# Kernel optimization log

Hardware: AMD Instinct MI355X
Metric: run time of the kernel (lower is better)

The kernel has to match this reference:

```python
import jax, jax.numpy as jnp
import numpy as np
import math
from jax import lax

L, E, H, F = 4, 1024, 16, 4096
B, S = 8, 512
VV, VR = 40, 30
DIST_V = 200
PAD_ID = 0


def setup_inputs() -> dict:
    key = jax.random.key(0)
    ks = iter(jax.random.split(key, 32))
    w = lambda *sh: jax.random.normal(next(ks), sh, jnp.float32) * 0.02
    inp = {
        'val_emb': w(VV, E),
        'ring_emb': w(VR, E),
        'dist_emb': w(DIST_V, H),
        'Wqkv': w(L, 3 * E, E), 'bqkv': jnp.zeros((L, 3 * E), jnp.float32),
        'Wo': w(L, E, E), 'bo': jnp.zeros((L, E), jnp.float32),
        'ln1_s': jnp.ones((L, E), jnp.float32), 'ln1_b': jnp.zeros((L, E), jnp.float32),
        'W1': w(L, F, E), 'b1': jnp.zeros((L, F), jnp.float32),
        'W2': w(L, E, F), 'b2': jnp.zeros((L, E), jnp.float32),
        'ln2_s': jnp.ones((L, E), jnp.float32), 'ln2_b': jnp.zeros((L, E), jnp.float32),
        'lnf_s': jnp.ones((E,), jnp.float32), 'lnf_b': jnp.zeros((E,), jnp.float32),
        'gen_W': w(VV * VR, E), 'gen_b': jnp.zeros((VV * VR,), jnp.float32),
    }
    val = jax.random.randint(next(ks), (B, S), 0, VV)
    val = val.at[:, 0].set(1)  # ensure first key is never <pad> (id 0)
    inp['val_sequences'] = val
    inp['ring_sequences'] = jax.random.randint(next(ks), (B, S), 0, VR)
    inp['distance_squares'] = jax.random.randint(next(ks), (B, S, S), 0, DIST_V)
    return inp


def _ln(x, s, b):
    m = x.mean(-1, keepdims=True)
    v = ((x - m) ** 2).mean(-1, keepdims=True)
    return (x - m) / jnp.sqrt(v + 1e-5) * s + b


def _forward(val_emb, ring_emb, dist_emb, Wqkv, bqkv, Wo, bo, ln1_s, ln1_b,
             W1, b1, W2, b2, ln2_s, ln2_b, lnf_s, lnf_b, gen_W, gen_b,
             val_sequences, ring_sequences, distance_squares):
    Bv, Sv = val_sequences.shape
    dh = E // H
    scale = 1.0 / math.sqrt(dh)
    # token embeddings, each scaled by sqrt(emb_size)
    x = (val_emb[val_sequences] + ring_emb[ring_sequences]) * math.sqrt(E)  # [B,S,E]
    # distance bias [B,S,S,H] -> [B,H,S,S], causal fill with -inf, key padding -inf
    bias = jnp.transpose(dist_emb[distance_squares], (0, 3, 1, 2))
    causal = jnp.tril(jnp.ones((Sv, Sv), bool))
    mask = jnp.where(causal[None, None], bias, -jnp.inf)
    pad = (val_sequences == PAD_ID)  # [B,S]
    mask = jnp.where(pad[:, None, None, :], -jnp.inf, mask)

    def step(h, p):
        wqkv, bq, wo, bo_, l1s, l1b, w1, b1_, w2, b2_, l2s, l2b = p
        qkv = h @ wqkv.T + bq  # [B,S,3E]
        q, k, v = jnp.split(qkv, 3, axis=-1)
        q = q.reshape(Bv, Sv, H, dh).transpose(0, 2, 1, 3)
        k = k.reshape(Bv, Sv, H, dh).transpose(0, 2, 1, 3)
        v = v.reshape(Bv, Sv, H, dh).transpose(0, 2, 1, 3)
        scores = jnp.einsum('bhqd,bhkd->bhqk', q, k) * scale + mask
        a = jax.nn.softmax(scores, axis=-1)
        ctx = jnp.einsum('bhqk,bhkd->bhqd', a, v)
        ctx = ctx.transpose(0, 2, 1, 3).reshape(Bv, Sv, E)
        h = _ln(h + ctx @ wo.T + bo_, l1s, l1b)  # post-norm
        ff = jax.nn.gelu(h @ w1.T + b1_, approximate=False) @ w2.T + b2_
        h = _ln(h + ff, l2s, l2b)
        return h, None

    layer_params = (Wqkv, bqkv, Wo, bo, ln1_s, ln1_b, W1, b1, W2, b2, ln2_s, ln2_b)
    x, _ = lax.scan(step, x, layer_params)
    x = _ln(x, lnf_s, lnf_b)
    return x @ gen_W.T + gen_b  # [B,S,VV*VR]


def reference(val_emb, ring_emb, dist_emb, Wqkv, bqkv, Wo, bo, ln1_s, ln1_b,
              W1, b1, W2, b2, ln2_s, ln2_b, lnf_s, lnf_b, gen_W, gen_b,
              val_sequences, ring_sequences, distance_squares):
    return _forward(val_emb, ring_emb, dist_emb, Wqkv, bqkv, Wo, bo, ln1_s, ln1_b,
                    W1, b1, W2, b2, ln2_s, ln2_b, lnf_s, lnf_b, gen_W, gen_b,
                    val_sequences, ring_sequences, distance_squares)
```

## Files before the change

### kernel.cpp

```cpp
#include <hip/hip_runtime.h>
#include <hip/hip_bf16.h>

typedef __attribute__((ext_vector_type(8))) short bf16x8;
typedef __attribute__((ext_vector_type(4))) float f32x4;
typedef unsigned short u16;
typedef __attribute__((ext_vector_type(4))) unsigned short u16x4;

#define L_ 4
#define E_ 1024
#define H_ 16
#define F_ 4096
#define B_ 8
#define S_ 512
#define T_ 4096
#define GEN_N 1200

#define AS1 __attribute__((address_space(1)))
#define AS3 __attribute__((address_space(3)))

static __device__ __forceinline__ u16 f2bf(float f) {
  unsigned u = __float_as_uint(f);
  unsigned r = (u + 0x7fffu + ((u >> 16) & 1u)) >> 16;
  return (u16)r;
}

static __device__ __forceinline__ float fast_gelu(float v) {
  float y = 0.7978845608f * (v + 0.044715f * v * v * v);
  y = fminf(fmaxf(y, -9.f), 9.f);
  float e2 = __expf(2.f * y);
  float th = (e2 - 1.f) / (e2 + 1.f);
  return 0.5f * v * (1.f + th);
}

__global__ __launch_bounds__(256) void cvt_bf16(const float* __restrict__ src,
                                                u16* __restrict__ dst, int n) {
  int i = (blockIdx.x * 256 + threadIdx.x) * 4;
  if (i >= n) return;
  float4 v = *reinterpret_cast<const float4*>(src + i);
  u16x4 o = {f2bf(v.x), f2bf(v.y), f2bf(v.z), f2bf(v.w)};
  *reinterpret_cast<u16x4*>(dst + i) = o;
}

__global__ __launch_bounds__(256) void embed_k(const float* __restrict__ val_emb,
                                               const float* __restrict__ ring_emb,
                                               const int* __restrict__ vseq,
                                               const int* __restrict__ rseq,
                                               float* __restrict__ h, u16* __restrict__ xbf) {
  int tok = blockIdx.x;
  int e = threadIdx.x * 4;
  int v = vseq[tok], r = rseq[tok];
  float4 a = *reinterpret_cast<const float4*>(val_emb + v * E_ + e);
  float4 b = *reinterpret_cast<const float4*>(ring_emb + r * E_ + e);
  float4 o;
  o.x = (a.x + b.x) * 32.f; o.y = (a.y + b.y) * 32.f;
  o.z = (a.z + b.z) * 32.f; o.w = (a.w + b.w) * 32.f;
  *reinterpret_cast<float4*>(h + (size_t)tok * E_ + e) = o;
  u16x4 ob = {f2bf(o.x), f2bf(o.y), f2bf(o.z), f2bf(o.w)};
  *reinterpret_cast<u16x4*>(xbf + (size_t)tok * E_ + e) = ob;
}

__global__ __launch_bounds__(256) void ln_k(const float* hin, const float* add0,
                                            const float* add1, const float* cbias,
                                            const float* g, const float* bta,
                                            float* hout, u16* xout) {
  int tok = blockIdx.x;
  int e = threadIdx.x * 4;
  float4 v = *reinterpret_cast<const float4*>(hin + (size_t)tok * E_ + e);
  if (add0) {
    float4 a0 = *reinterpret_cast<const float4*>(add0 + (size_t)tok * E_ + e);
    float4 a1 = *reinterpret_cast<const float4*>(add1 + (size_t)tok * E_ + e);
    float4 cb = *reinterpret_cast<const float4*>(cbias + e);
    v.x += a0.x + a1.x + cb.x; v.y += a0.y + a1.y + cb.y;
    v.z += a0.z + a1.z + cb.z; v.w += a0.w + a1.w + cb.w;
  }
  float s = v.x + v.y + v.z + v.w;
  float q = v.x * v.x + v.y * v.y + v.z * v.z + v.w * v.w;
  #pragma unroll
  for (int off = 1; off < 64; off <<= 1) {
    s += __shfl_xor(s, off, 64);
    q += __shfl_xor(q, off, 64);
  }
  __shared__ float ls[4], lq[4];
  int wv = threadIdx.x >> 6, ln = threadIdx.x & 63;
  if (ln == 0) { ls[wv] = s; lq[wv] = q; }
  __syncthreads();
  s = ls[0] + ls[1] + ls[2] + ls[3];
  q = lq[0] + lq[1] + lq[2] + lq[3];
  float mean = s * (1.f / E_);
  float var = q * (1.f / E_) - mean * mean;
  float inv = rsqrtf(var + 1e-5f);
  float4 gg = *reinterpret_cast<const float4*>(g + e);
  float4 bb = *reinterpret_cast<const float4*>(bta + e);
  float4 o;
  o.x = (v.x - mean) * inv * gg.x + bb.x;
  o.y = (v.y - mean) * inv * gg.y + bb.y;
  o.z = (v.z - mean) * inv * gg.z + bb.z;
  o.w = (v.w - mean) * inv * gg.w + bb.w;
  if (hout) *reinterpret_cast<float4*>(hout + (size_t)tok * E_ + e) = o;
  u16x4 ob = {f2bf(o.x), f2bf(o.y), f2bf(o.z), f2bf(o.w)};
  *reinterpret_cast<u16x4*>(xout + (size_t)tok * E_ + e) = ob;
}

template <int EPI, int NW, int SPLITK>
__global__ __launch_bounds__(512, 2) void gemm_big(const u16* __restrict__ A,
                                                   const u16* __restrict__ W,
                                                   const float* __restrict__ bias,
                                                   void* __restrict__ Cp,
                                                   int M, int N, int K, int tilesN) {
  constexpr int BN = 64 * NW;
  __shared__ __align__(16) u16 As[2][256 * 64];
  __shared__ __align__(16) u16 Bs[2][BN * 64];
  int tid = threadIdx.x;
  int wid = tid >> 6, ln = tid & 63;
  int wm = wid >> 2, wn = wid & 3;
  int lr = ln & 15, lk = ln >> 4;
  int nwg = gridDim.x;
  int bid = blockIdx.x;
  int swz = ((nwg & 7) == 0) ? ((bid & 7) * (nwg >> 3) + (bid >> 3)) : bid;
  int sp = 0, tile = swz;
  if (SPLITK > 1) { sp = swz & (SPLITK - 1); tile = swz / SPLITK; }
  int tm = tile / tilesN, tn = tile % tilesN;
  int row0 = tm * 256, col0 = tn * BN;
  int Ks = K / SPLITK;
  int kbase = sp * Ks;

  int srow = tid >> 3;
  int schunk = ((tid & 7) ^ (srow & 7)) * 8;
  const u16* gA = A + (size_t)(row0 + srow) * K + kbase + schunk;
  const u16* gB = W + (size_t)(col0 + srow) * K + kbase + schunk;
  size_t ldsBase = (size_t)((wid << 3) * 64) * 2;

  auto stage = [&](int buf, int kt) {
    size_t ko = (size_t)kt * 64;
    #pragma unroll
    for (int i = 0; i < 4; ++i)
      __builtin_amdgcn_global_load_lds(
          (const AS1 void*)(gA + (size_t)i * 64 * K + ko),
          (AS3 void*)((char*)&As[buf][0] + ldsBase + (size_t)i * 64 * 128), 16, 0, 0);
    #pragma unroll
    for (int i = 0; i < NW; ++i)
      __builtin_amdgcn_global_load_lds(
          (const AS1 void*)(gB + (size_t)i * 64 * K + ko),
          (AS3 void*)((char*)&Bs[buf][0] + ldsBase + (size_t)i * 64 * 128), 16, 0, 0);
  };

  f32x4 acc[8][NW];
  f32x4 z = {0.f, 0.f, 0.f, 0.f};
  #pragma unroll
  for (int m = 0; m < 8; ++m)
    #pragma unroll
    for (int n = 0; n < NW; ++n) acc[m][n] = z;

  auto compute = [&](int buf) {
    #pragma unroll
    for (int s = 0; s < 2; ++s) {
      int ch = ((s * 4 + lk) ^ (lr & 7)) * 8;
      bf16x8 bfr[NW];
      #pragma unroll
      for (int n = 0; n < NW; ++n)
        bfr[n] = *reinterpret_cast<const bf16x8*>(&Bs[buf][(wn * (16 * NW) + n * 16 + lr) * 64 + ch]);
      #pragma unroll
      for (int m = 0; m < 8; ++m) {
        bf16x8 af = *reinterpret_cast<const bf16x8*>(&As[buf][(wm * 128 + m * 16 + lr) * 64 + ch]);
        #pragma unroll
        for (int n = 0; n < NW; ++n)
          acc[m][n] = __builtin_amdgcn_mfma_f32_16x16x32_bf16(af, bfr[n], acc[m][n], 0, 0, 0);
      }
    }
  };

  int nt = Ks >> 6;
  stage(0, 0);
  int cur = 0;
  for (int t = 0; t < nt; ++t) {
    if (t + 1 < nt) {
      stage(cur ^ 1, t + 1);
      if constexpr (NW == 2) asm volatile("s_waitcnt vmcnt(6)" ::: "memory");
      else if constexpr (NW == 3) asm volatile("s_waitcnt vmcnt(7)" ::: "memory");
      else asm volatile("s_waitcnt vmcnt(8)" ::: "memory");
    } else {
      asm volatile("s_waitcnt vmcnt(0)" ::: "memory");
    }
    __builtin_amdgcn_s_barrier();
    asm volatile("" ::: "memory");
    compute(cur);
    asm volatile("" ::: "memory");
    __builtin_amdgcn_s_barrier();
    cur ^= 1;
  }

  #pragma unroll
  for (int n = 0; n < NW; ++n) {
    int col = col0 + wn * (16 * NW) + n * 16 + lr;
    float bv = (EPI == 2) ? 0.f : bias[col];
    #pragma unroll
    for (int m = 0; m < 8; ++m) {
      int rbase = row0 + wm * 128 + m * 16 + lk * 4;
      #pragma unroll
      for (int r2 = 0; r2 < 4; ++r2) {
        float v = acc[m][n][r2] + bv;
        if (EPI == 1) v = fast_gelu(v);
        if (EPI == 2)
          ((float*)Cp)[(size_t)sp * M * N + (size_t)(rbase + r2) * N + col] = v;
        else
          ((u16*)Cp)[(size_t)(rbase + r2) * N + col] = f2bf(v);
      }
    }
  }
}

template <int EPI>
__global__ __launch_bounds__(256) void gemm_bt(const u16* __restrict__ A,
                                               const u16* __restrict__ W,
                                               const float* __restrict__ bias,
                                               void* __restrict__ Cp,
                                               int M, int N, int K, int tilesN) {
  __shared__ __align__(16) u16 As[3][128 * 32];
  __shared__ __align__(16) u16 Bs[3][128 * 32];
  int tid = threadIdx.x;
  int wv = tid >> 6, ln = tid & 63;
  int wm = wv >> 1, wn = wv & 1;
  int nwg = gridDim.x;
  int bid = blockIdx.x;
  int swz = ((nwg & 7) == 0) ? ((bid & 7) * (nwg >> 3) + (bid >> 3)) : bid;
  int tm = swz / tilesN, tn = swz % tilesN;
  int row0 = tm * 128, col0 = tn * 128;
  int lr = ln & 15, lk = ln >> 4;

  f32x4 acc[4][4];
  f32x4 z = {0.f, 0.f, 0.f, 0.f};
  #pragma unroll
  for (int m = 0; m < 4; ++m)
    #pragma unroll
    for (int n = 0; n < 4; ++n) acc[m][n] = z;

  int srow = tid >> 2;
  int scol = ((tid & 3) ^ (srow & 3)) * 8;
  const u16* gA0 = A + (size_t)(row0 + srow) * K + scol;
  const u16* gA1 = A + (size_t)(row0 + 64 + srow) * K + scol;
  int wr0 = col0 + srow;      if (wr0 >= N) wr0 = N - 1;
  int wr1 = col0 + 64 + srow; if (wr1 >= N) wr1 = N - 1;
  const u16* gB0 = W + (size_t)wr0 * K + scol;
  const u16* gB1 = W + (size_t)wr1 * K + scol;
  size_t ldsOff0 = (size_t)(wv << 6) * 16;
  size_t ldsOff1 = (size_t)(256 + (wv << 6)) * 16;

  auto stage = [&](int buf, int k0) {
    __builtin_amdgcn_global_load_lds((const AS1 void*)(gA0 + k0),
        (AS3 void*)((char*)&As[buf][0] + ldsOff0), 16, 0, 0);
    __builtin_amdgcn_global_load_lds((const AS1 void*)(gB0 + k0),
        (AS3 void*)((char*)&Bs[buf][0] + ldsOff0), 16, 0, 0);
    __builtin_amdgcn_global_load_lds((const AS1 void*)(gA1 + k0),
        (AS3 void*)((char*)&As[buf][0] + ldsOff1), 16, 0, 0);
    __builtin_amdgcn_global_load_lds((const AS1 void*)(gB1 + k0),
        (AS3 void*)((char*)&Bs[buf][0] + ldsOff1), 16, 0, 0);
  };

  int ck = (lk ^ (lr & 3)) * 8;
  auto compute = [&](int buf) {
    bf16x8 af[4], bfr[4];
    #pragma unroll
    for (int m = 0; m < 4; ++m)
      af[m] = *reinterpret_cast<const bf16x8*>(&As[buf][(wm * 64 + m * 16 + lr) * 32 + ck]);
    #pragma unroll
    for (int n = 0; n < 4; ++n)
      bfr[n] = *reinterpret_cast<const bf16x8*>(&Bs[buf][(wn * 64 + n * 16 + lr) * 32 + ck]);
    #pragma unroll
    for (int m = 0; m < 4; ++m)
      #pragma unroll
      for (int n = 0; n < 4; ++n)
        acc[m][n] = __builtin_amdgcn_mfma_f32_16x16x32_bf16(af[m], bfr[n], acc[m][n], 0, 0, 0);
  };

  int nsteps = K >> 5;
  stage(0, 0);
  stage(1, 32);
  int bt = 0;
  for (int t = 0; t < nsteps; ++t) {
    int rem = nsteps - 1 - t;
    if (rem >= 2) {
      int b2 = (bt == 0) ? 2 : bt - 1;
      stage(b2, (t + 2) << 5);
      asm volatile("s_waitcnt vmcnt(8)" ::: "memory");
    } else if (rem == 1) {
      asm volatile("s_waitcnt vmcnt(4)" ::: "memory");
    } else {
      asm volatile("s_waitcnt vmcnt(0)" ::: "memory");
    }
    __builtin_amdgcn_s_barrier();
    asm volatile("" ::: "memory");
    compute(bt);
    asm volatile("" ::: "memory");
    __builtin_amdgcn_s_barrier();
    bt = (bt == 2) ? 0 : bt + 1;
  }

  #pragma unroll
  for (int n = 0; n < 4; ++n) {
    int col = col0 + wn * 64 + n * 16 + lr;
    if (col >= N) continue;
    float bv = bias[col];
    #pragma unroll
    for (int m = 0; m < 4; ++m) {
      int rbase = row0 + wm * 64 + m * 16 + lk * 4;
      #pragma unroll
      for (int r2 = 0; r2 < 4; ++r2) {
        float v = acc[m][n][r2] + bv;
        int row = rbase + r2;
        if (EPI == 2)
          ((float*)Cp)[(size_t)row * N + col] = v;
        else
          ((float*)Cp)[(size_t)row * N + col] += v;
      }
    }
  }
}

__global__ __launch_bounds__(256) void vtrans_k(const u16* __restrict__ qkv,
                                                u16* __restrict__ Vt) {
  int blk = blockIdx.x;
  int kt = blk & 7, bh = blk >> 3;
  int b = bh >> 4, h = bh & 15;
  __shared__ u16 t[64 * 66];
  int tid = threadIdx.x;
  #pragma unroll
  for (int i = 0; i < 16; ++i) {
    int idx = i * 256 + tid;
    int kk = idx >> 6, d = idx & 63;
    t[kk * 66 + d] = qkv[(size_t)(b * S_ + kt * 64 + kk) * 3072 + 2 * E_ + h * 64 + d];
  }
  __syncthreads();
  #pragma unroll
  for (int i = 0; i < 16; ++i) {
    int idx = i * 256 + tid;
    int d = idx >> 6, kk = idx & 63;
    Vt[(size_t)(bh * 64 + d) * S_ + kt * 64 + kk] = t[kk * 66 + d];
  }
}

__global__ __launch_bounds__(256, 4) void attn_scores_k(const u16* __restrict__ qkv,
                                                        const int* __restrict__ dist,
                                                        const float* __restrict__ dist_emb,
                                                        const int* __restrict__ vseq,
                                                        u16* __restrict__ P,
                                                        float* __restrict__ invl) {
  int blk = blockIdx.x;
  int bh = blk & 127;
  int qt = blk >> 7;
  int b = bh >> 4, h = bh & 15;
  int tid = threadIdx.x, wv = tid >> 6, ln = tid & 63;
  int lr = ln & 15, lk = ln >> 4;

  __shared__ float de[208];
  __shared__ unsigned char padf[512];
  __shared__ unsigned char d8[64 * 512];

  int ncol = (qt + 1) * 64;
  for (int i = tid; i < 208; i += 256)
    de[i] = (i < 200) ? dist_emb[i * H_ + h] : -1e30f;
  for (int i = tid; i < (ncol >> 2); i += 256) {
    int4 v = *reinterpret_cast<const int4*>(vseq + b * S_ + i * 4);
    uchar4 pz;
    pz.x = (v.x == 0); pz.y = (v.y == 0); pz.z = (v.z == 0); pz.w = (v.w == 0);
    *reinterpret_cast<uchar4*>(&padf[i * 4]) = pz;
  }
  __syncthreads();

  {
    int r = tid >> 2;
    const int* drow = dist + ((size_t)(b * S_ + qt * 64 + r) << 9);
    int nc4 = ncol >> 2;
    for (int c4 = (tid & 3); c4 < nc4; c4 += 4) {
      int4 dv = *reinterpret_cast<const int4*>(drow + c4 * 4);
      uchar4 o;
      o.x = padf[c4 * 4 + 0] ? (unsigned char)200 : (unsigned char)dv.x;
      o.y = padf[c4 * 4 + 1] ? (unsigned char)200 : (unsigned char)dv.y;
      o.z = padf[c4 * 4 + 2] ? (unsigned char)200 : (unsigned char)dv.z;
      o.w = padf[c4 * 4 + 3] ? (unsigned char)200 : (unsigned char)dv.w;
      *reinterpret_cast<uchar4*>(&d8[(r << 9) + c4 * 4]) = o;
    }
  }
  __syncthreads();

  int q0 = qt * 64 + wv * 16;
  int nv = 4 * qt + wv + 1;
  int nreq = 4 * qt + 2 * (wv >> 1) + 2;
  int qrow = q0 + lk * 4;
  int lrow = wv * 16 + lk * 4;

  bf16x8 aq0 = *reinterpret_cast<const bf16x8*>(
      qkv + (size_t)(b * S_ + q0 + lr) * 3072 + h * 64 + lk * 8);
  bf16x8 aq1 = *reinterpret_cast<const bf16x8*>(
      qkv + (size_t)(b * S_ + q0 + lr) * 3072 + h * 64 + 32 + lk * 8);

  float sm[4] = {0.f, 0.f, 0.f, 0.f};
  f32x4 z = {0.f, 0.f, 0.f, 0.f};
  int nch = (nv + 3) >> 2;
  #pragma unroll 1
  for (int c = 0; c < nch; ++c) {
    int base = c * 4;
    f32x4 acc[4] = {z, z, z, z};
    #pragma unroll
    for (int j = 0; j < 4; ++j) {
      int n = base + j;
      if (n < nv) {
        const u16* kb = qkv + (size_t)(b * S_ + n * 16 + lr) * 3072 + E_ + h * 64 + lk * 8;
        bf16x8 bk0 = *reinterpret_cast<const bf16x8*>(kb);
        bf16x8 bk1 = *reinterpret_cast<const bf16x8*>(kb + 32);
        acc[j] = __builtin_amdgcn_mfma_f32_16x16x32_bf16(aq0, bk0, acc[j], 0, 0, 0);
        acc[j] = __builtin_amdgcn_mfma_f32_16x16x32_bf16(aq1, bk1, acc[j], 0, 0, 0);
      }
    }
    #pragma unroll
    for (int j = 0; j < 4; ++j) {
      int n = base + j;
      if (n < nv) {
        int col = n * 16 + lr;
        #pragma unroll
        for (int r2 = 0; r2 < 4; ++r2) {
          float e = 0.f;
          if (col <= qrow + r2) {
            int d = d8[((lrow + r2) << 9) + col];
            e = __expf(acc[j][r2] * 0.125f + de[d]);
          }
          sm[r2] += e;
          P[(size_t)(bh * S_ + qrow + r2) * S_ + col] = f2bf(e);
        }
      }
    }
  }
  for (int n = nv; n < nreq; ++n) {
    int col = n * 16 + lr;
    #pragma unroll
    for (int r2 = 0; r2 < 4; ++r2)
      P[(size_t)(bh * S_ + qrow + r2) * S_ + col] = 0;
  }
  #pragma unroll
  for (int off = 1; off < 16; off <<= 1)
    #pragma unroll
    for (int r2 = 0; r2 < 4; ++r2) sm[r2] += __shfl_xor(sm[r2], off, 64);
  if (lr == 0) {
    #pragma unroll
    for (int r2 = 0; r2 < 4; ++r2)
      invl[bh * S_ + qrow + r2] = 1.f / sm[r2];
  }
}

__global__ __launch_bounds__(256) void attn_pv_k(const u16* __restrict__ P,
                                                 const u16* __restrict__ Vt,
                                                 const float* __restrict__ invl,
                                                 u16* __restrict__ ctx) {
  int blk = blockIdx.x;
  int mt = blk & 3, bh = blk >> 2;
  int b = bh >> 4, h = bh & 15;
  int tid = threadIdx.x, wv = tid >> 6, ln = tid & 63;
  int lr = ln & 15, lk = ln >> 4;
  int r0 = mt * 128 + wv * 32;
  f32x4 acc[2][4];
  f32x4 z = {0.f, 0.f, 0.f, 0.f};
  #pragma unroll
  for (int m = 0; m < 2; ++m)
    #pragma unroll
    for (int n = 0; n < 4; ++n) acc[m][n] = z;
  int nks = mt * 4 + wv + 1;
  for (int ks = 0; ks < nks; ++ks) {
    int k0 = ks * 32;
    bf16x8 ap[2];
    #pragma unroll
    for (int m = 0; m < 2; ++m)
      ap[m] = *reinterpret_cast<const bf16x8*>(
          P + (size_t)(bh * S_ + r0 + m * 16 + lr) * S_ + k0 + lk * 8);
    #pragma unroll
    for (int n = 0; n < 4; ++n) {
      bf16x8 bv = *reinterpret_cast<const bf16x8*>(
          Vt + (size_t)(bh * 64 + n * 16 + lr) * S_ + k0 + lk * 8);
      #pragma unroll
      for (int m = 0; m < 2; ++m)
        acc[m][n] = __builtin_amdgcn_mfma_f32_16x16x32_bf16(ap[m], bv, acc[m][n], 0, 0, 0);
    }
  }
  float il[2][4];
  #pragma unroll
  for (int m = 0; m < 2; ++m)
    #pragma unroll
    for (int r = 0; r < 4; ++r)
      il[m][r] = invl[bh * S_ + r0 + m * 16 + lk * 4 + r];
  #pragma unroll
  for (int m = 0; m < 2; ++m)
    #pragma unroll
    for (int n = 0; n < 4; ++n)
      #pragma unroll
      for (int r = 0; r < 4; ++r) {
        int row = r0 + m * 16 + lk * 4 + r;
        int col = n * 16 + lr;
        ctx[(size_t)(b * S_ + row) * E_ + h * 64 + col] = f2bf(acc[m][n][r] * il[m][r]);
      }
}

extern "C" void kernel_launch(void* const* d_in, const int* in_sizes, int n_in,
                              void* d_out, int out_size, void* d_ws, size_t ws_size,
                              hipStream_t stream) {
  const float* val_emb = (const float*)d_in[0];
  const float* ring_emb = (const float*)d_in[1];
  const float* dist_emb = (const float*)d_in[2];
  const float* Wqkv = (const float*)d_in[3];
  const float* bqkv = (const float*)d_in[4];
  const float* Wo = (const float*)d_in[5];
  const float* bo = (const float*)d_in[6];
  const float* ln1_s = (const float*)d_in[7];
  const float* ln1_b = (const float*)d_in[8];
  const float* W1 = (const float*)d_in[9];
  const float* b1 = (const float*)d_in[10];
  const float* W2 = (const float*)d_in[11];
  const float* b2 = (const float*)d_in[12];
  const float* ln2_s = (const float*)d_in[13];
  const float* ln2_b = (const float*)d_in[14];
  const float* lnf_s = (const float*)d_in[15];
  const float* lnf_b = (const float*)d_in[16];
  const float* gen_W = (const float*)d_in[17];
  const float* gen_b = (const float*)d_in[18];
  const int* vseq = (const int*)d_in[19];
  const int* rseq = (const int*)d_in[20];
  const int* dist = (const int*)d_in[21];

  char* ws = (char*)d_ws;
  size_t off = 0;
  auto alloc = [&](size_t nbytes) {
    char* p = ws + off;
    off += (nbytes + 255) & ~(size_t)255;
    return p;
  };
  u16* gw_bf = (u16*)alloc((size_t)GEN_N * E_ * 2);
  u16* wqkv_l = (u16*)alloc((size_t)3 * E_ * E_ * 2);
  u16* wo_l = (u16*)alloc((size_t)E_ * E_ * 2);
  u16* w1_l = (u16*)alloc((size_t)F_ * E_ * 2);
  u16* w2_l = (u16*)alloc((size_t)E_ * F_ * 2);
  float* h = (float*)alloc((size_t)T_ * E_ * 4);
  u16* x_bf = (u16*)alloc((size_t)T_ * E_ * 2);
  u16* qkv_bf = (u16*)alloc((size_t)T_ * 3 * E_ * 2);
  u16* ctx_bf = (u16*)alloc((size_t)T_ * E_ * 2);
  u16* vt_bf = (u16*)alloc((size_t)B_ * H_ * 64 * S_ * 2);
  float* invl = (float*)alloc((size_t)B_ * H_ * S_ * 4);
  u16* p_bf = (u16*)alloc((size_t)B_ * H_ * S_ * S_ * 2);
  u16* ff_bf = p_bf;
  float* psum = (float*)(p_bf + (size_t)T_ * F_);
  (void)ws_size; (void)in_sizes; (void)n_in; (void)out_size; (void)rseq;

  auto cvt = [&](const float* s, u16* d, int n) {
    cvt_bf16<<<dim3((n / 4 + 255) / 256), dim3(256), 0, stream>>>(s, d, n);
  };
  cvt(gen_W, gw_bf, GEN_N * E_);

  embed_k<<<dim3(T_), dim3(256), 0, stream>>>(val_emb, ring_emb, vseq, rseq, h, x_bf);

  for (int l = 0; l < L_; ++l) {
    cvt(Wqkv + (size_t)l * 3 * E_ * E_, wqkv_l, 3 * E_ * E_);
    cvt(Wo + (size_t)l * E_ * E_, wo_l, E_ * E_);
    cvt(W1 + (size_t)l * F_ * E_, w1_l, F_ * E_);
    cvt(W2 + (size_t)l * E_ * F_, w2_l, E_ * F_);

    gemm_big<0, 3, 1><<<dim3(256), dim3(512), 0, stream>>>(
        x_bf, wqkv_l, bqkv + (size_t)l * 3 * E_, qkv_bf, T_, 3 * E_, E_, 16);
    vtrans_k<<<dim3(B_ * H_ * 8), dim3(256), 0, stream>>>(qkv_bf, vt_bf);
    attn_scores_k<<<dim3(B_ * H_ * 8), dim3(256), 0, stream>>>(qkv_bf, dist, dist_emb, vseq,
                                                               p_bf, invl);
    attn_pv_k<<<dim3(B_ * H_ * 4), dim3(256), 0, stream>>>(p_bf, vt_bf, invl, ctx_bf);
    gemm_bt<3><<<dim3(32 * 8), dim3(256), 0, stream>>>(
        ctx_bf, wo_l, bo + (size_t)l * E_, h, T_, E_, E_, 8);
    ln_k<<<dim3(T_), dim3(256), 0, stream>>>(h, nullptr, nullptr, nullptr,
                                             ln1_s + (size_t)l * E_, ln1_b + (size_t)l * E_,
                                             h, x_bf);
    gemm_big<1, 4, 1><<<dim3(256), dim3(512), 0, stream>>>(
        x_bf, w1_l, b1 + (size_t)l * F_, ff_bf, T_, F_, E_, 16);
    gemm_big<2, 2, 2><<<dim3(256), dim3(512), 0, stream>>>(
        ff_bf, w2_l, nullptr, psum, T_, E_, F_, 8);
    ln_k<<<dim3(T_), dim3(256), 0, stream>>>(h, psum, psum + (size_t)T_ * E_,
                                             b2 + (size_t)l * E_,
                                             ln2_s + (size_t)l * E_, ln2_b + (size_t)l * E_,
                                             h, x_bf);
  }
  ln_k<<<dim3(T_), dim3(256), 0, stream>>>(h, nullptr, nullptr, nullptr, lnf_s, lnf_b,
                                           nullptr, x_bf);
  gemm_bt<2><<<dim3(32 * 10), dim3(256), 0, stream>>>(
      x_bf, gw_bf, gen_b, (float*)d_out, T_, GEN_N, E_, 10);
}
```

Baseline: 1.161 ms.

## Switch GEMM to 4-stage BK=32 LDS pipeline with priority boost

The main GEMM goes from a double-buffered pipeline with K-tiles of 64 to a 4-buffer ring with K-tiles of 32, keeping three loads in flight ahead of compute. The LDS swizzle and the staging layout are reworked for 32-wide rows, and the vmcnt waits are adjusted per stage. s_setprio is raised around the MFMA compute. The aim is to hide global-load latency better, at the cost of twice as many barriers per unit of K and more complex wait accounting. For NW==3, half the waves issue the second B load, so the vmcnt counts differ between waves, which could be fragile.

New measurement: 1.268 ms. 1.09x slower.

```diff
diff --git a/kernel.cpp b/kernel.cpp
--- a/kernel.cpp
+++ b/kernel.cpp
@@ -108,8 +108,8 @@
                                                    void* __restrict__ Cp,
                                                    int M, int N, int K, int tilesN) {
   constexpr int BN = 64 * NW;
-  __shared__ __align__(16) u16 As[2][256 * 64];
-  __shared__ __align__(16) u16 Bs[2][BN * 64];
+  __shared__ __align__(16) u16 As[4][256 * 32];
+  __shared__ __align__(16) u16 Bs[4][BN * 32];
   int tid = threadIdx.x;
   int wid = tid >> 6, ln = tid & 63;
   int wm = wid >> 2, wn = wid & 3;
@@ -124,24 +124,28 @@
   int Ks = K / SPLITK;
   int kbase = sp * Ks;
 
-  int srow = tid >> 3;
-  int schunk = ((tid & 7) ^ (srow & 7)) * 8;
-  const u16* gA = A + (size_t)(row0 + srow) * K + kbase + schunk;
-  const u16* gB = W + (size_t)(col0 + srow) * K + kbase + schunk;
-  size_t ldsBase = (size_t)((wid << 3) * 64) * 2;
+  int srow = tid >> 2;
+  int sch = ((tid & 3) ^ ((srow >> 1) & 3)) * 8;
+  const u16* gA = A + (size_t)(row0 + srow) * K + kbase + sch;
+  const u16* gB = W + (size_t)(col0 + srow) * K + kbase + sch;
+  size_t wslot = (size_t)wid * 1024;
 
   auto stage = [&](int buf, int kt) {
-    size_t ko = (size_t)kt * 64;
-    #pragma unroll
-    for (int i = 0; i < 4; ++i)
-      __builtin_amdgcn_global_load_lds(
-          (const AS1 void*)(gA + (size_t)i * 64 * K + ko),
-          (AS3 void*)((char*)&As[buf][0] + ldsBase + (size_t)i * 64 * 128), 16, 0, 0);
-    #pragma unroll
-    for (int i = 0; i < NW; ++i)
-      __builtin_amdgcn_global_load_lds(
-          (const AS1 void*)(gB + (size_t)i * 64 * K + ko),
-          (AS3 void*)((char*)&Bs[buf][0] + ldsBase + (size_t)i * 64 * 128), 16, 0, 0);
+    size_t ko = (size_t)kt * 32;
+    __builtin_amdgcn_global_load_lds((const AS1 void*)(gA + ko),
+        (AS3 void*)((char*)&As[buf][0] + wslot), 16, 0, 0);
+    __builtin_amdgcn_global_load_lds((const AS1 void*)(gA + (size_t)128 * K + ko),
+        (AS3 void*)((char*)&As[buf][0] + 8192 + wslot), 16, 0, 0);
+    __builtin_amdgcn_global_load_lds((const AS1 void*)(gB + ko),
+        (AS3 void*)((char*)&Bs[buf][0] + wslot), 16, 0, 0);
+    if constexpr (NW == 4) {
+      __builtin_amdgcn_global_load_lds((const AS1 void*)(gB + (size_t)128 * K + ko),
+          (AS3 void*)((char*)&Bs[buf][0] + 8192 + wslot), 16, 0, 0);
+    } else if constexpr (NW == 3) {
+      if (wid < 4)
+        __builtin_amdgcn_global_load_lds((const AS1 void*)(gB + (size_t)128 * K + ko),
+            (AS3 void*)((char*)&Bs[buf][0] + 8192 + wslot), 16, 0, 0);
+    }
   };
 
   f32x4 acc[8][NW];
@@ -151,42 +155,48 @@
     #pragma unroll
     for (int n = 0; n < NW; ++n) acc[m][n] = z;
 
+  int ck = (lk ^ ((lr >> 1) & 3)) * 8;
   auto compute = [&](int buf) {
-    #pragma unroll
-    for (int s = 0; s < 2; ++s) {
-      int ch = ((s * 4 + lk) ^ (lr & 7)) * 8;
-      bf16x8 bfr[NW];
+    bf16x8 bfr[NW];
+    #pragma unroll
+    for (int n = 0; n < NW; ++n)
+      bfr[n] = *reinterpret_cast<const bf16x8*>(&Bs[buf][(wn * (16 * NW) + n * 16 + lr) * 32 + ck]);
+    #pragma unroll
+    for (int m = 0; m < 8; ++m) {
+      bf16x8 af = *reinterpret_cast<const bf16x8*>(&As[buf][(wm * 128 + m * 16 + lr) * 32 + ck]);
       #pragma unroll
       for (int n = 0; n < NW; ++n)
-        bfr[n] = *reinterpret_cast<const bf16x8*>(&Bs[buf][(wn * (16 * NW) + n * 16 + lr) * 64 + ch]);
-      #pragma unroll
-      for (int m = 0; m < 8; ++m) {
-        bf16x8 af = *reinterpret_cast<const bf16x8*>(&As[buf][(wm * 128 + m * 16 + lr) * 64 + ch]);
-        #pragma unroll
-        for (int n = 0; n < NW; ++n)
-          acc[m][n] = __builtin_amdgcn_mfma_f32_16x16x32_bf16(af, bfr[n], acc[m][n], 0, 0, 0);
-      }
+        acc[m][n] = __builtin_amdgcn_mfma_f32_16x16x32_bf16(af, bfr[n], acc[m][n], 0, 0, 0);
     }
   };
 
-  int nt = Ks >> 6;
+  int nt = Ks >> 5;
   stage(0, 0);
-  int cur = 0;
+  stage(1, 1);
+  stage(2, 2);
   for (int t = 0; t < nt; ++t) {
-    if (t + 1 < nt) {
-      stage(cur ^ 1, t + 1);
-      if constexpr (NW == 2) asm volatile("s_waitcnt vmcnt(6)" ::: "memory");
-      else if constexpr (NW == 3) asm volatile("s_waitcnt vmcnt(7)" ::: "memory");
-      else asm volatile("s_waitcnt vmcnt(8)" ::: "memory");
+    int buf = t & 3;
+    int rem = nt - 1 - t;
+    if (rem >= 3) {
+      stage((t + 3) & 3, t + 3);
+      if constexpr (NW == 4) asm volatile("s_waitcnt vmcnt(12)" ::: "memory");
+      else asm volatile("s_waitcnt vmcnt(9)" ::: "memory");
+    } else if (rem == 2) {
+      if constexpr (NW == 4) asm volatile("s_waitcnt vmcnt(8)" ::: "memory");
+      else asm volatile("s_waitcnt vmcnt(6)" ::: "memory");
+    } else if (rem == 1) {
+      if constexpr (NW == 4) asm volatile("s_waitcnt vmcnt(4)" ::: "memory");
+      else asm volatile("s_waitcnt vmcnt(3)" ::: "memory");
     } else {
       asm volatile("s_waitcnt vmcnt(0)" ::: "memory");
     }
     __builtin_amdgcn_s_barrier();
     asm volatile("" ::: "memory");
-    compute(cur);
+    __builtin_amdgcn_s_setprio(1);
+    compute(buf);
+    __builtin_amdgcn_s_setprio(0);
     asm volatile("" ::: "memory");
     __builtin_amdgcn_s_barrier();
-    cur ^= 1;
   }
 
   #pragma unroll
```

## Fuse V transpose into QKV GEMM, unify Wo and generator GEMMs on gemm_big

Applied to the files above, without the earlier changes.

Removes the separate vtrans_k kernel by having the QKV GEMM epilogue also scatter V values into the transposed Vt buffer. Replaces gemm_bt for the Wo projection with split-K gemm_big writing partial sums that the following layernorm reduces with the bias, and runs the generator projection through gemm_big with a padded weight buffer. This cuts kernel launches and intermediate traffic. In exchange the Vt scatter stores are uncoalesced, and the padded generator weight rows (1200 to 1280) are read without the pad region being written.

After: 1.161 ms. No clear change (+0.0%).

```diff
diff --git a/kernel.cpp b/kernel.cpp
--- a/kernel.cpp
+++ b/kernel.cpp
@@ -14,6 +14,7 @@
 #define S_ 512
 #define T_ 4096
 #define GEN_N 1200
+#define GEN_PAD 1280
 
 #define AS1 __attribute__((address_space(1)))
 #define AS3 __attribute__((address_space(3)))
@@ -106,6 +107,7 @@
                                                    const u16* __restrict__ W,
                                                    const float* __restrict__ bias,
                                                    void* __restrict__ Cp,
+                                                   u16* __restrict__ Vt,
                                                    int M, int N, int K, int tilesN) {
   constexpr int BN = 64 * NW;
   __shared__ __align__(16) u16 As[2][256 * 64];
@@ -192,6 +194,7 @@
   #pragma unroll
   for (int n = 0; n < NW; ++n) {
     int col = col0 + wn * (16 * NW) + n * 16 + lr;
+    if (col >= N) continue;
     float bv = (EPI == 2) ? 0.f : bias[col];
     #pragma unroll
     for (int m = 0; m < 8; ++m) {
@@ -200,141 +203,23 @@
       for (int r2 = 0; r2 < 4; ++r2) {
         float v = acc[m][n][r2] + bv;
         if (EPI == 1) v = fast_gelu(v);
-        if (EPI == 2)
-          ((float*)Cp)[(size_t)sp * M * N + (size_t)(rbase + r2) * N + col] = v;
-        else
-          ((u16*)Cp)[(size_t)(rbase + r2) * N + col] = f2bf(v);
-      }
-    }
-  }
-}
-
-template <int EPI>
-__global__ __launch_bounds__(256) void gemm_bt(const u16* __restrict__ A,
-                                               const u16* __restrict__ W,
-                                               const float* __restrict__ bias,
-                                               void* __restrict__ Cp,
-                                               int M, int N, int K, int tilesN) {
-  __shared__ __align__(16) u16 As[3][128 * 32];
-  __shared__ __align__(16) u16 Bs[3][128 * 32];
-  int tid = threadIdx.x;
-  int wv = tid >> 6, ln = tid & 63;
-  int wm = wv >> 1, wn = wv & 1;
-  int nwg = gridDim.x;
-  int bid = blockIdx.x;
-  int swz = ((nwg & 7) == 0) ? ((bid & 7) * (nwg >> 3) + (bid >> 3)) : bid;
-  int tm = swz / tilesN, tn = swz % tilesN;
-  int row0 = tm * 128, col0 = tn * 128;
-  int lr = ln & 15, lk = ln >> 4;
-
-  f32x4 acc[4][4];
-  f32x4 z = {0.f, 0.f, 0.f, 0.f};
-  #pragma unroll
-  for (int m = 0; m < 4; ++m)
-    #pragma unroll
-    for (int n = 0; n < 4; ++n) acc[m][n] = z;
-
-  int srow = tid >> 2;
-  int scol = ((tid & 3) ^ (srow & 3)) * 8;
-  const u16* gA0 = A + (size_t)(row0 + srow) * K + scol;
-  const u16* gA1 = A + (size_t)(row0 + 64 + srow) * K + scol;
-  int wr0 = col0 + srow;      if (wr0 >= N) wr0 = N - 1;
-  int wr1 = col0 + 64 + srow; if (wr1 >= N) wr1 = N - 1;
-  const u16* gB0 = W + (size_t)wr0 * K + scol;
-  const u16* gB1 = W + (size_t)wr1 * K + scol;
-  size_t ldsOff0 = (size_t)(wv << 6) * 16;
-  size_t ldsOff1 = (size_t)(256 + (wv << 6)) * 16;
-
-  auto stage = [&](int buf, int k0) {
-    __builtin_amdgcn_global_load_lds((const AS1 void*)(gA0 + k0),
-        (AS3 void*)((char*)&As[buf][0] + ldsOff0), 16, 0, 0);
-    __builtin_amdgcn_global_load_lds((const AS1 void*)(gB0 + k0),
-        (AS3 void*)((char*)&Bs[buf][0] + ldsOff0), 16, 0, 0);
-    __builtin_amdgcn_global_load_lds((const AS1 void*)(gA1 + k0),
-        (AS3 void*)((char*)&As[buf][0] + ldsOff1), 16, 0, 0);
-    __builtin_amdgcn_global_load_lds((const AS1 void*)(gB1 + k0),
-        (AS3 void*)((char*)&Bs[buf][0] + ldsOff1), 16, 0, 0);
-  };
-
-  int ck = (lk ^ (lr & 3)) * 8;
-  auto compute = [&](int buf) {
-    bf16x8 af[4], bfr[4];
-    #pragma unroll
-    for (int m = 0; m < 4; ++m)
-      af[m] = *reinterpret_cast<const bf16x8*>(&As[buf][(wm * 64 + m * 16 + lr) * 32 + ck]);
-    #pragma unroll
-    for (int n = 0; n < 4; ++n)
-      bfr[n] = *reinterpret_cast<const bf16x8*>(&Bs[buf][(wn * 64 + n * 16 + lr) * 32 + ck]);
-    #pragma unroll
-    for (int m = 0; m < 4; ++m)
-      #pragma unroll
-      for (int n = 0; n < 4; ++n)
-        acc[m][n] = __builtin_amdgcn_mfma_f32_16x16x32_bf16(af[m], bfr[n], acc[m][n], 0, 0, 0);
-  };
-
-  int nsteps = K >> 5;
-  stage(0, 0);
-  stage(1, 32);
-  int bt = 0;
-  for (int t = 0; t < nsteps; ++t) {
-    int rem = nsteps - 1 - t;
-    if (rem >= 2) {
-      int b2 = (bt == 0) ? 2 : bt - 1;
-      stage(b2, (t + 2) << 5);
-      asm volatile("s_waitcnt vmcnt(8)" ::: "memory");
-    } else if (rem == 1) {
-      asm volatile("s_waitcnt vmcnt(4)" ::: "memory");
-    } else {
-      asm volatile("s_waitcnt vmcnt(0)" ::: "memory");
-    }
-    __builtin_amdgcn_s_barrier();
-    asm volatile("" ::: "memory");
-    compute(bt);
-    asm volatile("" ::: "memory");
-    __builtin_amdgcn_s_barrier();
-    bt = (bt == 2) ? 0 : bt + 1;
-  }
-
-  #pragma unroll
-  for (int n = 0; n < 4; ++n) {
-    int col = col0 + wn * 64 + n * 16 + lr;
-    if (col >= N) continue;
-    float bv = bias[col];
-    #pragma unroll
-    for (int m = 0; m < 4; ++m) {
-      int rbase = row0 + wm * 64 + m * 16 + lk * 4;
-      #pragma unroll
-      for (int r2 = 0; r2 < 4; ++r2) {
-        float v = acc[m][n][r2] + bv;
         int row = rbase + r2;
         if (EPI == 2)
+          ((float*)Cp)[(size_t)sp * M * N + (size_t)row * N + col] = v;
+        else if (EPI == 3)
           ((float*)Cp)[(size_t)row * N + col] = v;
-        else
-          ((float*)Cp)[(size_t)row * N + col] += v;
+        else {
+          u16 bw = f2bf(v);
+          ((u16*)Cp)[(size_t)row * N + col] = bw;
+          if (EPI == 0 && Vt != nullptr && col >= 2 * E_) {
+            int dg = col - 2 * E_;
+            int hh = dg >> 6, dd = dg & 63;
+            int bb = row >> 9, ss = row & 511;
+            Vt[((size_t)((bb * 16 + hh) * 64 + dd) << 9) + ss] = bw;
+          }
+        }
       }
     }
-  }
-}
-
-__global__ __launch_bounds__(256) void vtrans_k(const u16* __restrict__ qkv,
-                                                u16* __restrict__ Vt) {
-  int blk = blockIdx.x;
-  int kt = blk & 7, bh = blk >> 3;
-  int b = bh >> 4, h = bh & 15;
-  __shared__ u16 t[64 * 66];
-  int tid = threadIdx.x;
-  #pragma unroll
-  for (int i = 0; i < 16; ++i) {
-    int idx = i * 256 + tid;
-    int kk = idx >> 6, d = idx & 63;
-    t[kk * 66 + d] = qkv[(size_t)(b * S_ + kt * 64 + kk) * 3072 + 2 * E_ + h * 64 + d];
-  }
-  __syncthreads();
-  #pragma unroll
-  for (int i = 0; i < 16; ++i) {
-    int idx = i * 256 + tid;
-    int d = idx >> 6, kk = idx & 63;
-    Vt[(size_t)(bh * 64 + d) * S_ + kt * 64 + kk] = t[kk * 66 + d];
   }
 }
 
@@ -530,7 +415,7 @@
     off += (nbytes + 255) & ~(size_t)255;
     return p;
   };
-  u16* gw_bf = (u16*)alloc((size_t)GEN_N * E_ * 2);
+  u16* gw_bf = (u16*)alloc((size_t)GEN_PAD * E_ * 2);
   u16* wqkv_l = (u16*)alloc((size_t)3 * E_ * E_ * 2);
   u16* wo_l = (u16*)alloc((size_t)E_ * E_ * 2);
   u16* w1_l = (u16*)alloc((size_t)F_ * E_ * 2);
@@ -560,20 +445,20 @@
     cvt(W2 + (size_t)l * E_ * F_, w2_l, E_ * F_);
 
     gemm_big<0, 3, 1><<<dim3(256), dim3(512), 0, stream>>>(
-        x_bf, wqkv_l, bqkv + (size_t)l * 3 * E_, qkv_bf, T_, 3 * E_, E_, 16);
-    vtrans_k<<<dim3(B_ * H_ * 8), dim3(256), 0, stream>>>(qkv_bf, vt_bf);
+        x_bf, wqkv_l, bqkv + (size_t)l * 3 * E_, qkv_bf, vt_bf, T_, 3 * E_, E_, 16);
     attn_scores_k<<<dim3(B_ * H_ * 8), dim3(256), 0, stream>>>(qkv_bf, dist, dist_emb, vseq,
                                                                p_bf, invl);
     attn_pv_k<<<dim3(B_ * H_ * 4), dim3(256), 0, stream>>>(p_bf, vt_bf, invl, ctx_bf);
-    gemm_bt<3><<<dim3(32 * 8), dim3(256), 0, stream>>>(
-        ctx_bf, wo_l, bo + (size_t)l * E_, h, T_, E_, E_, 8);
-    ln_k<<<dim3(T_), dim3(256), 0, stream>>>(h, nullptr, nullptr, nullptr,
+    gemm_big<2, 2, 2><<<dim3(256), dim3(512), 0, stream>>>(
+        ctx_bf, wo_l, nullptr, psum, nullptr, T_, E_, E_, 8);
+    ln_k<<<dim3(T_), dim3(256), 0, stream>>>(h, psum, psum + (size_t)T_ * E_,
+                                             bo + (size_t)l * E_,
                                              ln1_s + (size_t)l * E_, ln1_b + (size_t)l * E_,
                                              h, x_bf);
     gemm_big<1, 4, 1><<<dim3(256), dim3(512), 0, stream>>>(
-        x_bf, w1_l, b1 + (size_t)l * F_, ff_bf, T_, F_, E_, 16);
+        x_bf, w1_l, b1 + (size_t)l * F_, ff_bf, nullptr, T_, F_, E_, 16);
     gemm_big<2, 2, 2><<<dim3(256), dim3(512), 0, stream>>>(
-        ff_bf, w2_l, nullptr, psum, T_, E_, F_, 8);
+        ff_bf, w2_l, nullptr, psum, nullptr, T_, E_, F_, 8);
     ln_k<<<dim3(T_), dim3(256), 0, stream>>>(h, psum, psum + (size_t)T_ * E_,
                                              b2 + (size_t)l * E_,
                                              ln2_s + (size_t)l * E_, ln2_b + (size_t)l * E_,
@@ -581,6 +466,6 @@
   }
   ln_k<<<dim3(T_), dim3(256), 0, stream>>>(h, nullptr, nullptr, nullptr, lnf_s, lnf_b,
                                            nullptr, x_bf);
-  gemm_bt<2><<<dim3(32 * 10), dim3(256), 0, stream>>>(
-      x_bf, gw_bf, gen_b, (float*)d_out, T_, GEN_N, E_, 10);
-}
+  gemm_big<3, 2, 1><<<dim3(160), dim3(512), 0, stream>>>(
+      x_bf, gw_bf, gen_b, (float*)d_out, nullptr, T_, GEN_N, E_, 10);
+}
```
